# Kernel optimization log

Measured on AMD Instinct MI355X. Metric: run time of the kernel, lower is better.

The kernel has to match this reference:

```python
import jax, jax.numpy as jnp
import numpy as np

BLANK_ID = 0


def setup_inputs() -> dict:
    key = jax.random.key(0)
    ks = jax.random.split(key, 8)
    B, T, H, V = 32, 1000, 640, 5000
    s = 0.02
    tn_output = jax.random.normal(ks[0], (B, T, H), dtype=jnp.float32)
    embed = jax.random.normal(ks[1], (V, H), dtype=jnp.float32) * s
    Wx = jax.random.normal(ks[2], (H, 4 * H), dtype=jnp.float32) * s  # LSTM input weights
    Wh = jax.random.normal(ks[3], (H, 4 * H), dtype=jnp.float32) * s  # LSTM recurrent weights
    b = jnp.zeros((4 * H,), dtype=jnp.float32)
    Wc = jax.random.normal(ks[4], (H, V), dtype=jnp.float32) * s     # classifier weights
    bc = jnp.zeros((V,), dtype=jnp.float32)
    return {"tn_output": tn_output, "embed": embed, "Wx": Wx, "Wh": Wh,
            "b": b, "Wc": Wc, "bc": bc}


def _lstm_step(tok, h, c, embed, Wx, Wh, b):
    # tok: [B] int32, h/c: [B,H]
    x = embed[tok]                                   # [B,H] gather (PN embedding)
    g = x @ Wx + h @ Wh + b                          # [B,4H]
    i, f, gg, o = jnp.split(g, 4, axis=-1)
    c2 = jax.nn.sigmoid(f) * c + jax.nn.sigmoid(i) * jnp.tanh(gg)
    h2 = jax.nn.sigmoid(o) * jnp.tanh(c2)
    return h2, c2


def reference(tn_output, embed, Wx, Wh, b, Wc, bc):
    """Batched transducer greedy decode (beam_size=1 path).
    Per t: joint = tanh(TN_t + out_PN); logits = joint @ Wc + bc; log_softmax;
    argmax; if != blank, emit token, accumulate logp, advance PN state (masked).
    Returns (logp_scores [B], predictions [B,T] with blank where no emission).
    """
    B, T, H = tn_output.shape
    tok0 = jnp.full((B,), BLANK_ID, dtype=jnp.int32)
    h0 = jnp.zeros((B, H), dtype=tn_output.dtype)
    c0 = jnp.zeros((B, H), dtype=tn_output.dtype)
    # initial PN forward on the blank token (hidden = None -> zeros)
    h, c = _lstm_step(tok0, h0, c0, embed, Wx, Wh, b)
    out_PN = h

    def step(carry, tn_t):
        h, c, out_PN, tok, scores = carry
        logits = jnp.tanh(tn_t + out_PN) @ Wc + bc            # joint ('sum') + classifier
        logp = jax.nn.log_softmax(logits, axis=-1)            # [B,V]
        pos = jnp.argmax(logp, axis=-1)                       # [B]
        val = jnp.max(logp, axis=-1)                          # [B]
        upd = pos != BLANK_ID
        scores = scores + jnp.where(upd, val, 0.0)
        new_tok = jnp.where(upd, pos.astype(jnp.int32), tok)
        h2, c2 = _lstm_step(new_tok, h, c, embed, Wx, Wh, b)
        m = upd[:, None]
        h = jnp.where(m, h2, h)
        c = jnp.where(m, c2, c)
        out_PN = jnp.where(m, h2, out_PN)
        emit = jnp.where(upd, pos, BLANK_ID).astype(jnp.int32)
        return (h, c, out_PN, new_tok, scores), emit

    carry0 = (h, c, out_PN, tok0, jnp.zeros((B,), dtype=tn_output.dtype))
    (h, c, out_PN, tok, scores), emits = jax.lax.scan(
        step, carry0, jnp.swapaxes(tn_output, 0, 1))          # scan over time
    preds = jnp.swapaxes(emits, 0, 1)                          # [B,T]
    return scores, preds
```

## Files before the change

kernel.cpp:

```cpp
#include <hip/hip_runtime.h>
#include <float.h>

#define BB 32
#define TT 1000
#define HH 640
#define H4 2560
#define VV 5000
#define NLOG 157
#define NGATE 80
#define NB   240

#define O_JOINT 0
#define O_HT    20480
#define O_PM    40960
#define O_PS    46080
#define O_PI    51200
#define O_BAR   56320
#define O_CT    56704
#define O_PNT   77184
#define O_XWXB  97664
#define XWXB_ELEMS ((size_t)VV * (size_t)H4)
#define O_WHP   (O_XWXB + 12800000)
#define WHP_ELEMS ((size_t)NGATE * HH * 32)

typedef unsigned int u32;
typedef unsigned long long u64;

__device__ __forceinline__ float sigf(float x) { return 1.0f / (1.0f + expf(-x)); }

__device__ __forceinline__ float ldc1(const float* p) {
  u32 v = __hip_atomic_load((const u32*)p, __ATOMIC_RELAXED, __HIP_MEMORY_SCOPE_AGENT);
  return __uint_as_float(v);
}
__device__ __forceinline__ void stc1(float* p, float x) {
  __hip_atomic_store((u32*)p, __float_as_uint(x), __ATOMIC_RELAXED, __HIP_MEMORY_SCOPE_AGENT);
}

__device__ __forceinline__ void stage_sc1_full(float* dst, const float* src, int tid) {
  const float* p0 = src + 4 * (tid + 0 * 512);
  const float* p1 = src + 4 * (tid + 1 * 512);
  const float* p2 = src + 4 * (tid + 2 * 512);
  const float* p3 = src + 4 * (tid + 3 * 512);
  const float* p4 = src + 4 * (tid + 4 * 512);
  const float* p5 = src + 4 * (tid + 5 * 512);
  const float* p6 = src + 4 * (tid + 6 * 512);
  const float* p7 = src + 4 * (tid + 7 * 512);
  const float* p8 = src + 4 * (tid + 8 * 512);
  const float* p9 = src + 4 * (tid + 9 * 512);
  float4 a0, a1, a2, a3, a4, a5, a6, a7, a8, a9;
  asm volatile(
      "global_load_dwordx4 %0, %10, off sc0 sc1\n\t"
      "global_load_dwordx4 %1, %11, off sc0 sc1\n\t"
      "global_load_dwordx4 %2, %12, off sc0 sc1\n\t"
      "global_load_dwordx4 %3, %13, off sc0 sc1\n\t"
      "global_load_dwordx4 %4, %14, off sc0 sc1\n\t"
      "global_load_dwordx4 %5, %15, off sc0 sc1\n\t"
      "global_load_dwordx4 %6, %16, off sc0 sc1\n\t"
      "global_load_dwordx4 %7, %17, off sc0 sc1\n\t"
      "global_load_dwordx4 %8, %18, off sc0 sc1\n\t"
      "global_load_dwordx4 %9, %19, off sc0 sc1\n\t"
      "s_waitcnt vmcnt(0)"
      : "=&v"(a0), "=&v"(a1), "=&v"(a2), "=&v"(a3), "=&v"(a4),
        "=&v"(a5), "=&v"(a6), "=&v"(a7), "=&v"(a8), "=&v"(a9)
      : "v"(p0), "v"(p1), "v"(p2), "v"(p3), "v"(p4),
        "v"(p5), "v"(p6), "v"(p7), "v"(p8), "v"(p9)
      : "memory");
  float4* d4 = (float4*)dst;
  d4[tid + 0 * 512] = a0;
  d4[tid + 1 * 512] = a1;
  d4[tid + 2 * 512] = a2;
  d4[tid + 3 * 512] = a3;
  d4[tid + 4 * 512] = a4;
  d4[tid + 5 * 512] = a5;
  d4[tid + 6 * 512] = a6;
  d4[tid + 7 * 512] = a7;
  d4[tid + 8 * 512] = a8;
  d4[tid + 9 * 512] = a9;
}

__device__ __forceinline__ void grid_bar(unsigned* bar, unsigned target) {
  __syncthreads();
  if (threadIdx.x == 0) {
    const int g = (int)blockIdx.x / 30;
    unsigned* cnt  = bar + g * 16;
    unsigned* gen  = bar + (9 + g) * 16;
    asm volatile("s_waitcnt vmcnt(0)" ::: "memory");
    unsigned a = __hip_atomic_fetch_add(cnt, 1u, __ATOMIC_RELAXED, __HIP_MEMORY_SCOPE_AGENT);
    if (a == 29u) {
      unsigned* root = bar + 8 * 16;
      unsigned r = __hip_atomic_fetch_add(root, 1u, __ATOMIC_RELAXED, __HIP_MEMORY_SCOPE_AGENT);
      if (r == 7u) {
        __hip_atomic_store(root, 0u, __ATOMIC_RELAXED, __HIP_MEMORY_SCOPE_AGENT);
#pragma unroll
        for (int i = 0; i < 8; ++i)
          __hip_atomic_store(bar + i * 16, 0u, __ATOMIC_RELAXED, __HIP_MEMORY_SCOPE_AGENT);
        asm volatile("s_waitcnt vmcnt(0)" ::: "memory");
#pragma unroll
        for (int i = 0; i < 8; ++i)
          __hip_atomic_store(bar + (9 + i) * 16, target, __ATOMIC_RELAXED, __HIP_MEMORY_SCOPE_AGENT);
      }
    }
    while (__hip_atomic_load(gen, __ATOMIC_RELAXED, __HIP_MEMORY_SCOPE_AGENT) < target)
      __builtin_amdgcn_s_sleep(1);
  }
  __syncthreads();
}

__global__ __launch_bounds__(256) void precompute_k(const float* __restrict__ embed,
                                                    const float* __restrict__ Wx,
                                                    const float* __restrict__ bias,
                                                    float* __restrict__ xwxb) {
  __shared__ float embT[HH * 17];
  const int tid = threadIdx.x;
  const int v0 = blockIdx.y * 16;
  const int c0 = blockIdx.x * 256 + (tid & 63) * 4;
  const int vg = tid >> 6;
  for (int i = tid; i < 16 * 160; i += 256) {
    int vr = i / 160, kq = i - vr * 160;
    int v = v0 + vr; if (v >= VV) v = VV - 1;
    float4 e = *(const float4*)&embed[(size_t)v * HH + kq * 4];
    embT[(kq * 4 + 0) * 17 + vr] = e.x;
    embT[(kq * 4 + 1) * 17 + vr] = e.y;
    embT[(kq * 4 + 2) * 17 + vr] = e.z;
    embT[(kq * 4 + 3) * 17 + vr] = e.w;
  }
  __syncthreads();
  float acc[16];
#pragma unroll
  for (int i = 0; i < 16; ++i) acc[i] = 0.f;
#pragma unroll 4
  for (int k = 0; k < HH; ++k) {
    float4 wv = *(const float4*)&Wx[(size_t)k * H4 + c0];
#pragma unroll
    for (int i = 0; i < 4; ++i) {
      float e = embT[k * 17 + vg * 4 + i];
      acc[i * 4 + 0] += e * wv.x;
      acc[i * 4 + 1] += e * wv.y;
      acc[i * 4 + 2] += e * wv.z;
      acc[i * 4 + 3] += e * wv.w;
    }
  }
  float4 bv = *(const float4*)&bias[c0];
#pragma unroll
  for (int i = 0; i < 4; ++i) {
    int v = v0 + vg * 4 + i;
    if (v < VV) {
      float4 r;
      r.x = acc[i * 4 + 0] + bv.x; r.y = acc[i * 4 + 1] + bv.y;
      r.z = acc[i * 4 + 2] + bv.z; r.w = acc[i * 4 + 3] + bv.w;
      *(float4*)&xwxb[(size_t)v * H4 + c0] = r;
    }
  }
}

__global__ __launch_bounds__(256) void repack_k(const float* __restrict__ Wh,
                                                float* __restrict__ whp) {
  const int q = blockIdx.x;
  for (int i = threadIdx.x; i < HH * 32; i += 256) {
    int k = i >> 5, lc = i & 31;
    whp[((size_t)q * HH + k) * 32 + lc] =
        Wh[(size_t)k * H4 + (lc >> 3) * HH + q * 8 + (lc & 7)];
  }
}

__global__ __launch_bounds__(256) void init_k(const float* __restrict__ tn,
                                              const float* __restrict__ embed,
                                              const float* __restrict__ Wx,
                                              const float* __restrict__ bias,
                                              float* ws, int use_table) {
  const int tid = threadIdx.x, bid = blockIdx.x;
  const int b = tid & 31, c8 = tid >> 5;
  const int j = bid * 8 + c8;
  if (bid == 0) {
    unsigned* bar = (unsigned*)(ws + O_BAR);
    for (int i = tid; i < 17 * 16; i += 256) bar[i] = 0u;
  }
  const float* xwxb = ws + O_XWXB;
  float g4[4];
  if (use_table) {
#pragma unroll
    for (int g = 0; g < 4; ++g) g4[g] = xwxb[g * HH + j];
  } else {
#pragma unroll
    for (int g = 0; g < 4; ++g) g4[g] = bias[g * HH + j];
#pragma unroll 4
    for (int k = 0; k < HH; ++k) {
      float xv = embed[k];
#pragma unroll
      for (int g = 0; g < 4; ++g) g4[g] += xv * Wx[(size_t)k * H4 + g * HH + j];
    }
  }
  float c1 = sigf(g4[0]) * tanhf(g4[2]);
  float h1 = sigf(g4[3]) * tanhf(c1);
  ws[O_CT + j * 32 + b] = c1;
  ws[O_HT + j * 32 + b] = h1;
  ws[O_PNT + j * 32 + b] = h1;
  ws[O_JOINT + j * 32 + b] = tanhf(tn[(size_t)b * TT * HH + j] + h1);
}

__global__ __launch_bounds__(512) void decode_k(const float* __restrict__ tn,
                                                const float* __restrict__ embed,
                                                const float* __restrict__ Wx,
                                                const float* __restrict__ bias,
                                                const float* __restrict__ Wh,
                                                const float* __restrict__ Wc,
                                                const float* __restrict__ bc,
                                                float* __restrict__ out,
                                                float* ws, int use_table, int use_pack) {
  __shared__ float joint_s[20480];
  __shared__ float smem[10800];
  __shared__ float hwh_s[1056];
  __shared__ float c_s[256];
  __shared__ float pn_s[256];
  __shared__ int s_tok[32];
  __shared__ int s_upd[32];
  __shared__ int s_ptok[32];
  __shared__ float s_scores[32];
  const int tid = threadIdx.x, bid = blockIdx.x;
  unsigned* bar = (unsigned*)(ws + O_BAR);
  const float* xwxb = ws + O_XWXB;
  const bool is_log = (bid < NLOG);
  const bool is_gate = (bid >= NLOG) && (bid < NLOG + NGATE);
  const int q = bid - NLOG;

  if (tid < 32) { s_ptok[tid] = 0; s_scores[tid] = 0.f; }
  if (is_gate && tid < 256) {
    const int jj = tid >> 5, b = tid & 31;
    c_s[jj * 32 + b] = ws[O_CT + (q * 8 + jj) * 32 + b];
    pn_s[jj * 32 + b] = ws[O_PNT + (q * 8 + jj) * 32 + b];
  }
  __syncthreads();

  const int lane = tid & 63, wvv = tid >> 6;
  const int sub = lane >> 5;
  const int cg  = lane & 3;
  const int bg  = (lane >> 2) & 7;
  const int kb  = (wvv * 2 + sub) * 40;
  const float* wbase;
  int wstride;
  if (is_log) {
    int c = bid * 32 + cg * 8;
    if (c > VV - 8) c = VV - 8;
    wbase = Wc + (size_t)kb * VV + c;
    wstride = VV;
  } else if (use_pack) {
    wbase = ws + O_WHP + ((size_t)q * HH + kb) * 32 + cg * 8;
    wstride = 32;
  } else {
    wbase = Wh + (size_t)kb * H4 + cg * HH + q * 8;
    wstride = H4;
  }
  const float* jb0 = joint_s + kb * 32 + bg * 4;

  unsigned epoch = 0;
  for (int t = 0; t < TT; ++t) {
    float tnv = 0.f;

    if (is_log || is_gate) {
      if (is_gate && tid < 256 && t + 1 < TT)
        tnv = tn[((size_t)(tid & 31) * TT + (t + 1)) * HH + q * 8 + (tid >> 5)];
      stage_sc1_full(joint_s, ws + (is_log ? O_JOINT : O_HT), tid);
      __syncthreads();

      float acc[32];
#pragma unroll
      for (int i = 0; i < 32; ++i) acc[i] = 0.f;
      {
        const float* wp = wbase;
        const float* jp = jb0;
#pragma unroll 4
        for (int kk = 0; kk < 40; ++kk) {
          float4 w0 = *(const float4*)(wp);
          float4 w1 = *(const float4*)(wp + 4);
          float4 jv = *(const float4*)(jp);
          wp += wstride;
          jp += 32;
          acc[0]  += w0.x * jv.x; acc[1]  += w0.x * jv.y; acc[2]  += w0.x * jv.z; acc[3]  += w0.x * jv.w;
          acc[4]  += w0.y * jv.x; acc[5]  += w0.y * jv.y; acc[6]  += w0.y * jv.z; acc[7]  += w0.y * jv.w;
          acc[8]  += w0.z * jv.x; acc[9]  += w0.z * jv.y; acc[10] += w0.z * jv.z; acc[11] += w0.z * jv.w;
          acc[12] += w0.w * jv.x; acc[13] += w0.w * jv.y; acc[14] += w0.w * jv.z; acc[15] += w0.w * jv.w;
          acc[16] += w1.x * jv.x; acc[17] += w1.x * jv.y; acc[18] += w1.x * jv.z; acc[19] += w1.x * jv.w;
          acc[20] += w1.y * jv.x; acc[21] += w1.y * jv.y; acc[22] += w1.y * jv.z; acc[23] += w1.y * jv.w;
          acc[24] += w1.z * jv.x; acc[25] += w1.z * jv.y; acc[26] += w1.z * jv.z; acc[27] += w1.z * jv.w;
          acc[28] += w1.w * jv.x; acc[29] += w1.w * jv.y; acc[30] += w1.w * jv.z; acc[31] += w1.w * jv.w;
        }
      }
#pragma unroll
      for (int i = 0; i < 32; ++i) acc[i] += __shfl_xor(acc[i], 32);
      float* part = smem;
      if (sub == 0) {
        float* pb = part + wvv * 1152 + bg * 4;
#pragma unroll
        for (int c = 0; c < 8; ++c)
          *(float4*)&pb[(cg * 8 + c) * 36] =
              make_float4(acc[c * 4 + 0], acc[c * 4 + 1], acc[c * 4 + 2], acc[c * 4 + 3]);
      }
      __syncthreads();

      const int b = tid & 31, colg = tid >> 5;
      if (is_log) {
        float* lm = smem + 9216;
        float* lsv = smem + 9744;
        int* lix = (int*)(smem + 10272);
        float m = -FLT_MAX; int ix = 0;
        float lv[2];
#pragma unroll
        for (int i = 0; i < 2; ++i) {
          const int cl = colg * 2 + i;
          float s = 0.f;
#pragma unroll
          for (int qq = 0; qq < 8; ++qq) s += part[qq * 1152 + cl * 36 + b];
          int cgl = bid * 32 + cl;
          float l = (cgl < VV) ? s + bc[cgl] : -FLT_MAX;
          lv[i] = l;
          if (l > m) { m = l; ix = cgl; }
        }
        float e = 0.f;
        if (m > -FLT_MAX) {
#pragma unroll
          for (int i = 0; i < 2; ++i) e += expf(lv[i] - m);
        }
        lm[colg * 33 + b] = m; lsv[colg * 33 + b] = e; lix[colg * 33 + b] = ix;
        __syncthreads();
        if (tid < 32) {
          float m2 = lm[tid], s2 = lsv[tid]; int ix2 = lix[tid];
#pragma unroll
          for (int qq = 1; qq < 16; ++qq) {
            float M = lm[qq * 33 + tid], S = lsv[qq * 33 + tid]; int I = lix[qq * 33 + tid];
            if (M > m2) { s2 = s2 * expf(m2 - M) + S; m2 = M; ix2 = I; }
            else if (M > -FLT_MAX) { s2 += S * expf(M - m2); }
          }
          stc1(&ws[O_PM + bid * 32 + tid], m2);
          stc1(&ws[O_PS + bid * 32 + tid], s2);
          stc1(&ws[O_PI + bid * 32 + tid], __int_as_float(ix2));
        }
      } else {
#pragma unroll
        for (int i = 0; i < 2; ++i) {
          const int cl = colg * 2 + i;
          float s = 0.f;
#pragma unroll
          for (int qq = 0; qq < 8; ++qq) s += part[qq * 1152 + cl * 36 + b];
          hwh_s[cl * 33 + b] = s;
        }
      }
    }
    epoch++;
    grid_bar(bar, epoch);

    if (is_gate) {
      float* rm = smem;
      float* rs = smem + 528;
      int* ri = (int*)(smem + 1056);
      float* gmat = smem + 1584;
      float* xl = smem + 2640;
      const int r = tid & 31, c16 = tid >> 5;
      {
        float m = -FLT_MAX, s = 0.f; int ix = 0;
#pragma unroll
        for (int i = 0; i < 10; ++i) {
          int idx = c16 * 10 + i;
          bool v = (idx < NLOG);
          int ic = v ? idx : 0;
          float M = ldc1(&ws[O_PM + ic * 32 + r]);
          float S = ldc1(&ws[O_PS + ic * 32 + r]);
          int I = __float_as_int(ldc1(&ws[O_PI + ic * 32 + r]));
          if (!v) { M = -FLT_MAX; S = 0.f; I = 0; }
          if (M > m) { s = s * expf(m - M) + S; m = M; ix = I; }
          else if (M > -FLT_MAX) { s += S * expf(M - m); }
        }
        rm[c16 * 33 + r] = m; rs[c16 * 33 + r] = s; ri[c16 * 33 + r] = ix;
      }
      __syncthreads();
      if (tid < 32) {
        float m = rm[tid], s = rs[tid]; int ix = ri[tid];
#pragma unroll
        for (int qq = 1; qq < 16; ++qq) {
          float M = rm[qq * 33 + tid], S = rs[qq * 33 + tid]; int I = ri[qq * 33 + tid];
          if (M > m) { s = s * expf(m - M) + S; m = M; ix = I; }
          else { s += S * expf(M - m); }
        }
        int pos = ix;
        int upd = (pos != 0) ? 1 : 0;
        int ntk = upd ? pos : s_ptok[tid];
        s_tok[tid] = ntk; s_upd[tid] = upd; s_ptok[tid] = ntk;
        if (bid == NLOG) {
          float sc = s_scores[tid];
          if (upd) sc -= logf(s);
          s_scores[tid] = sc;
          out[BB + (size_t)tid * TT + t] = upd ? (float)pos : 0.0f;
          if (t == TT - 1) out[tid] = sc;
        }
      }
      __syncthreads();

      const int b = tid & 31;
      float gv[2];
#pragma unroll
      for (int h = 0; h < 2; ++h) {
        int lc = (tid >> 5) + h * 16;
        int wcol = (lc >> 3) * HH + q * 8 + (lc & 7);
        float v = hwh_s[lc * 33 + b];
        if (use_table) v += xwxb[(size_t)s_tok[b] * H4 + wcol];
        else v += bias[wcol];
        gv[h] = v;
      }
      if (!use_table) {
        for (int st = 0; st < 4; ++st) {
          const int k0 = st * 160;
          __syncthreads();
          for (int i = tid; i < 32 * 160; i += 512) {
            int bb = i / 160, kk = i - bb * 160;
            xl[bb * 161 + kk] = embed[(size_t)s_tok[bb] * HH + k0 + kk];
          }
          __syncthreads();
          for (int k = 0; k < 160; ++k) {
            float xv = xl[b * 161 + k];
#pragma unroll
            for (int h = 0; h < 2; ++h) {
              int lc = (tid >> 5) + h * 16;
              int wcol = (lc >> 3) * HH + q * 8 + (lc & 7);
              gv[h] += xv * Wx[(size_t)(k0 + k) * H4 + wcol];
            }
          }
        }
      }
#pragma unroll
      for (int h = 0; h < 2; ++h) {
        int lc = (tid >> 5) + h * 16;
        gmat[lc * 33 + b] = gv[h];
      }
      __syncthreads();
      if (tid < 256) {
        const int jj = tid >> 5, b2 = tid & 31;
        float gi = gmat[(0 * 8 + jj) * 33 + b2];
        float gf = gmat[(1 * 8 + jj) * 33 + b2];
        float gg = gmat[(2 * 8 + jj) * 33 + b2];
        float go = gmat[(3 * 8 + jj) * 33 + b2];
        float cold = c_s[jj * 32 + b2];
        float c2 = sigf(gf) * cold + sigf(gi) * tanhf(gg);
        float h2 = sigf(go) * tanhf(c2);
        float pv;
        if (s_upd[b2]) {
          c_s[jj * 32 + b2] = c2;
          pn_s[jj * 32 + b2] = h2;
          stc1(&ws[O_HT + (q * 8 + jj) * 32 + b2], h2);
          pv = h2;
        } else {
          pv = pn_s[jj * 32 + b2];
        }
        if (t + 1 < TT)
          stc1(&ws[O_JOINT + (q * 8 + jj) * 32 + b2], tanhf(tnv + pv));
      }
    }
    epoch++;
    grid_bar(bar, epoch);
  }
}

extern "C" void kernel_launch(void* const* d_in, const int* in_sizes, int n_in,
                              void* d_out, int out_size, void* d_ws, size_t ws_size,
                              hipStream_t stream) {
  const float* tn    = (const float*)d_in[0];
  const float* embed = (const float*)d_in[1];
  const float* Wx    = (const float*)d_in[2];
  const float* Wh    = (const float*)d_in[3];
  const float* bias  = (const float*)d_in[4];
  const float* Wc    = (const float*)d_in[5];
  const float* bc    = (const float*)d_in[6];
  float* out = (float*)d_out;
  float* ws  = (float*)d_ws;

  const size_t need_table = (size_t)(O_XWXB + XWXB_ELEMS) * sizeof(float);
  const size_t need_pack  = (size_t)(O_WHP + WHP_ELEMS) * sizeof(float);
  const int use_table = (ws_size >= need_table) ? 1 : 0;
  const int use_pack  = (ws_size >= need_pack) ? 1 : 0;

  if (use_table)
    hipLaunchKernelGGL(precompute_k, dim3(10, 313), dim3(256), 0, stream,
                       embed, Wx, bias, ws + O_XWXB);
  if (use_pack)
    hipLaunchKernelGGL(repack_k, dim3(NGATE), dim3(256), 0, stream, Wh, ws + O_WHP);
  hipLaunchKernelGGL(init_k, dim3(80), dim3(256), 0, stream, tn, embed, Wx, bias, ws, use_table);
  hipLaunchKernelGGL(decode_k, dim3(NB), dim3(512), 0, stream,
                     tn, embed, Wx, bias, Wh, Wc, bc, out, ws, use_table, use_pack);
}
```

Before: 23.75 ms.

## Use monotonic-counter grid barrier and nontemporal loads in persistent decode kernel

The grid barrier now uses monotonically increasing counters compared against multiples of the epoch, which removes the reset stores and the extra waitcnt on the critical path. Barrier counters are also spaced 128 bytes apart instead of 64. The gate blocks' Wh loads and the xwxb table gather become nontemporal loads to avoid polluting cache. The partial max/sum merge first issues all ten coherent loads before doing the online-softmax combine, so load latency can overlap. The risks are counter overflow over very long runs (not an issue for 1000 steps) and the workspace offsets moving.

```diff
diff --git a/kernel.cpp b/kernel.cpp
--- a/kernel.cpp
+++ b/kernel.cpp
@@ -16,15 +16,16 @@
 #define O_PS    46080
 #define O_PI    51200
 #define O_BAR   56320
-#define O_CT    56704
-#define O_PNT   77184
-#define O_XWXB  97664
+#define O_CT    56960
+#define O_PNT   77440
+#define O_XWXB  97920
 #define XWXB_ELEMS ((size_t)VV * (size_t)H4)
 #define O_WHP   (O_XWXB + 12800000)
 #define WHP_ELEMS ((size_t)NGATE * HH * 32)
 
 typedef unsigned int u32;
 typedef unsigned long long u64;
+typedef float vf4 __attribute__((ext_vector_type(4)));
 
 __device__ __forceinline__ float sigf(float x) { return 1.0f / (1.0f + expf(-x)); }
 
@@ -78,29 +79,24 @@
   d4[tid + 9 * 512] = a9;
 }
 
-__device__ __forceinline__ void grid_bar(unsigned* bar, unsigned target) {
+__device__ __forceinline__ void grid_bar(unsigned* bar, unsigned epoch) {
   __syncthreads();
   if (threadIdx.x == 0) {
     const int g = (int)blockIdx.x / 30;
-    unsigned* cnt  = bar + g * 16;
-    unsigned* gen  = bar + (9 + g) * 16;
+    unsigned* cnt = bar + g * 32;
+    unsigned* gen = bar + (9 + g) * 32;
     asm volatile("s_waitcnt vmcnt(0)" ::: "memory");
     unsigned a = __hip_atomic_fetch_add(cnt, 1u, __ATOMIC_RELAXED, __HIP_MEMORY_SCOPE_AGENT);
-    if (a == 29u) {
-      unsigned* root = bar + 8 * 16;
+    if (a == 30u * epoch - 1u) {
+      unsigned* root = bar + 8 * 32;
       unsigned r = __hip_atomic_fetch_add(root, 1u, __ATOMIC_RELAXED, __HIP_MEMORY_SCOPE_AGENT);
-      if (r == 7u) {
-        __hip_atomic_store(root, 0u, __ATOMIC_RELAXED, __HIP_MEMORY_SCOPE_AGENT);
+      if (r == 8u * epoch - 1u) {
 #pragma unroll
         for (int i = 0; i < 8; ++i)
-          __hip_atomic_store(bar + i * 16, 0u, __ATOMIC_RELAXED, __HIP_MEMORY_SCOPE_AGENT);
-        asm volatile("s_waitcnt vmcnt(0)" ::: "memory");
-#pragma unroll
-        for (int i = 0; i < 8; ++i)
-          __hip_atomic_store(bar + (9 + i) * 16, target, __ATOMIC_RELAXED, __HIP_MEMORY_SCOPE_AGENT);
+          __hip_atomic_store(bar + (9 + i) * 32, epoch, __ATOMIC_RELAXED, __HIP_MEMORY_SCOPE_AGENT);
       }
     }
-    while (__hip_atomic_load(gen, __ATOMIC_RELAXED, __HIP_MEMORY_SCOPE_AGENT) < target)
+    while (__hip_atomic_load(gen, __ATOMIC_RELAXED, __HIP_MEMORY_SCOPE_AGENT) < epoch)
       __builtin_amdgcn_s_sleep(1);
   }
   __syncthreads();
@@ -173,7 +169,7 @@
   const int j = bid * 8 + c8;
   if (bid == 0) {
     unsigned* bar = (unsigned*)(ws + O_BAR);
-    for (int i = tid; i < 17 * 16; i += 256) bar[i] = 0u;
+    for (int i = tid; i < 17 * 32; i += 256) bar[i] = 0u;
   }
   const float* xwxb = ws + O_XWXB;
   float g4[4];
@@ -265,7 +261,7 @@
       float acc[32];
 #pragma unroll
       for (int i = 0; i < 32; ++i) acc[i] = 0.f;
-      {
+      if (is_log) {
         const float* wp = wbase;
         const float* jp = jb0;
 #pragma unroll 4
@@ -284,6 +280,25 @@
           acc[24] += w1.z * jv.x; acc[25] += w1.z * jv.y; acc[26] += w1.z * jv.z; acc[27] += w1.z * jv.w;
           acc[28] += w1.w * jv.x; acc[29] += w1.w * jv.y; acc[30] += w1.w * jv.z; acc[31] += w1.w * jv.w;
         }
+      } else {
+        const float* wp = wbase;
+        const float* jp = jb0;
+#pragma unroll 4
+        for (int kk = 0; kk < 40; ++kk) {
+          vf4 w0 = __builtin_nontemporal_load((const vf4*)(wp));
+          vf4 w1 = __builtin_nontemporal_load((const vf4*)(wp + 4));
+          float4 jv = *(const float4*)(jp);
+          wp += wstride;
+          jp += 32;
+          acc[0]  += w0.x * jv.x; acc[1]  += w0.x * jv.y; acc[2]  += w0.x * jv.z; acc[3]  += w0.x * jv.w;
+          acc[4]  += w0.y * jv.x; acc[5]  += w0.y * jv.y; acc[6]  += w0.y * jv.z; acc[7]  += w0.y * jv.w;
+          acc[8]  += w0.z * jv.x; acc[9]  += w0.z * jv.y; acc[10] += w0.z * jv.z; acc[11] += w0.z * jv.w;
+          acc[12] += w0.w * jv.x; acc[13] += w0.w * jv.y; acc[14] += w0.w * jv.z; acc[15] += w0.w * jv.w;
+          acc[16] += w1.x * jv.x; acc[17] += w1.x * jv.y; acc[18] += w1.x * jv.z; acc[19] += w1.x * jv.w;
+          acc[20] += w1.y * jv.x; acc[21] += w1.y * jv.y; acc[22] += w1.y * jv.z; acc[23] += w1.y * jv.w;
+          acc[24] += w1.z * jv.x; acc[25] += w1.z * jv.y; acc[26] += w1.z * jv.z; acc[27] += w1.z * jv.w;
+          acc[28] += w1.w * jv.x; acc[29] += w1.w * jv.y; acc[30] += w1.w * jv.z; acc[31] += w1.w * jv.w;
+        }
       }
 #pragma unroll
       for (int i = 0; i < 32; ++i) acc[i] += __shfl_xor(acc[i], 32);
@@ -356,18 +371,22 @@
       float* xl = smem + 2640;
       const int r = tid & 31, c16 = tid >> 5;
       {
-        float m = -FLT_MAX, s = 0.f; int ix = 0;
+        float Ms[10], Ss[10]; int Is[10];
 #pragma unroll
         for (int i = 0; i < 10; ++i) {
           int idx = c16 * 10 + i;
           bool v = (idx < NLOG);
           int ic = v ? idx : 0;
-          float M = ldc1(&ws[O_PM + ic * 32 + r]);
-          float S = ldc1(&ws[O_PS + ic * 32 + r]);
-          int I = __float_as_int(ldc1(&ws[O_PI + ic * 32 + r]));
-          if (!v) { M = -FLT_MAX; S = 0.f; I = 0; }
-          if (M > m) { s = s * expf(m - M) + S; m = M; ix = I; }
-          else if (M > -FLT_MAX) { s += S * expf(M - m); }
+          Ms[i] = ldc1(&ws[O_PM + ic * 32 + r]);
+          Ss[i] = ldc1(&ws[O_PS + ic * 32 + r]);
+          Is[i] = __float_as_int(ldc1(&ws[O_PI + ic * 32 + r]));
+          if (!v) { Ms[i] = -FLT_MAX; Ss[i] = 0.f; Is[i] = 0; }
+        }
+        float m = -FLT_MAX, s = 0.f; int ix = 0;
+#pragma unroll
+        for (int i = 0; i < 10; ++i) {
+          if (Ms[i] > m) { s = s * expf(m - Ms[i]) + Ss[i]; m = Ms[i]; ix = Is[i]; }
+          else if (Ms[i] > -FLT_MAX) { s += Ss[i] * expf(Ms[i] - m); }
         }
         rm[c16 * 33 + r] = m; rs[c16 * 33 + r] = s; ri[c16 * 33 + r] = ix;
       }
@@ -401,7 +420,7 @@
         int lc = (tid >> 5) + h * 16;
         int wcol = (lc >> 3) * HH + q * 8 + (lc & 7);
         float v = hwh_s[lc * 33 + b];
-        if (use_table) v += xwxb[(size_t)s_tok[b] * H4 + wcol];
+        if (use_table) v += __builtin_nontemporal_load(&xwxb[(size_t)s_tok[b] * H4 + wcol]);
         else v += bias[wcol];
         gv[h] = v;
       }
```

After: 19.06 ms. 1.25x faster.
